# Performance work log

Measured on AMD Instinct MI355X. Metric: run time of the kernel, lower is better.

## Reference

```python
import jax, jax.numpy as jnp
import numpy as np

TOP_K = 2
NUM_MOE_LAYERS = 12


def _gemma_mlp(x, gate_w, up_w, down_w):
    # GemmaMLP: down( gelu_tanh(gate(x)) * up(x) )
    g = jnp.einsum('bsh,hi->bsi', x, gate_w)
    u = jnp.einsum('bsh,hi->bsi', x, up_w)
    return jnp.einsum('bsi,ih->bsh', jax.nn.gelu(g, approximate=True) * u, down_w)


def setup_inputs() -> dict:
    key = jax.random.key(0)
    ks = jax.random.split(key, 8)
    B, S, H, I, E = 32, 256, 1024, 4096, 8  # batch, seq, hidden, intermediate, skill experts
    std = 0.02
    return {
        'x': jax.random.normal(ks[0], (B, S, H), jnp.float32),
        'router_logits': jax.random.normal(ks[1], (B, E), jnp.float32),
        'skill_gate': jax.random.normal(ks[2], (E, H, I), jnp.float32) * std,
        'skill_up': jax.random.normal(ks[3], (E, H, I), jnp.float32) * std,
        'skill_down': jax.random.normal(ks[4], (E, I, H), jnp.float32) * std,
        'shared_gate': jax.random.normal(ks[5], (H, I), jnp.float32) * std,
        'shared_up': jax.random.normal(ks[6], (H, I), jnp.float32) * std,
        'shared_down': jax.random.normal(ks[7], (I, H), jnp.float32) * std,
    }


def reference(x, router_logits, skill_gate, skill_up, skill_down,
              shared_gate, shared_up, shared_down):
    B = x.shape[0]
    E = skill_gate.shape[0]
    # top-k softmax routing (per sequence), renormalized over selected experts
    rw = jax.nn.softmax(router_logits.astype(jnp.float32), axis=-1)
    w, sel = jax.lax.top_k(rw, TOP_K)                      # [B, k]
    w = w / w.sum(axis=-1, keepdims=True)
    w = w.astype(x.dtype)
    # ScaleGradient: identity fwd, grad scaled by 1/num_moe_layers
    scale = 1.0 / NUM_MOE_LAYERS
    w = scale * w + (1.0 - scale) * jax.lax.stop_gradient(w)
    # dense combine weights [B, E]; zero weight == not routed (same math as gather/scatter)
    dense_w = jnp.zeros((B, E), x.dtype).at[jnp.arange(B)[:, None], sel].add(w)

    def step(acc, params):
        g, u, d, we = params                               # we: [B]
        return acc + we[:, None, None] * _gemma_mlp(x, g, u, d), None

    out, _ = jax.lax.scan(step, jnp.zeros_like(x),
                          (skill_gate, skill_up, skill_down, dense_w.T))
    out = out + _gemma_mlp(x, shared_gate, shared_up, shared_down)
    return out
```

## Files before the change

kernel.cpp:

```cpp
#include <hip/hip_runtime.h>

typedef __bf16 bf16x8 __attribute__((ext_vector_type(8)));
typedef float  f32x4  __attribute__((ext_vector_type(4)));

__device__ __forceinline__ unsigned short f2bf(float f) {
    unsigned u = __float_as_uint(f);
    u += 0x7fffu + ((u >> 16) & 1u);
    return (unsigned short)(u >> 16);
}

__device__ __forceinline__ void gld_lds16(const void* g, void* l) {
    __builtin_amdgcn_global_load_lds(
        (const __attribute__((address_space(1))) void*)g,
        (__attribute__((address_space(3))) void*)l,
        16, 0, 0);
}

#define NB  32
#define SQ  256
#define HD  1024
#define ID  4096
#define NEXP 8
#define PAIRS (NB * 3)

#define OFF_EID    ((size_t)0)
#define OFF_WGT    ((size_t)512)
#define OFF_XBF    ((size_t)1024)
#define OFF_GATET  (OFF_XBF   + (size_t)16777216)
#define OFF_UPT    (OFF_GATET + (size_t)75497472)
#define OFF_DOWNT  (OFF_UPT   + (size_t)75497472)
#define OFF_ACT    (OFF_DOWNT + (size_t)75497472)

__global__ void routing_kernel(const float* __restrict__ logits,
                               int* __restrict__ eid, float* __restrict__ wgt) {
    int b = threadIdx.x;
    if (b < NB) {
        float l[NEXP];
        for (int j = 0; j < NEXP; ++j) l[j] = logits[b * NEXP + j];
        int a0 = 0;
        for (int j = 1; j < NEXP; ++j) if (l[j] > l[a0]) a0 = j;
        int a1 = -1;
        for (int j = 0; j < NEXP; ++j) {
            if (j == a0) continue;
            if (a1 < 0 || l[j] > l[a1]) a1 = j;
        }
        float w0 = 1.0f / (1.0f + expf(l[a1] - l[a0]));
        eid[b * 3 + 0] = a0;  wgt[b * 3 + 0] = w0;
        eid[b * 3 + 1] = a1;  wgt[b * 3 + 1] = 1.0f - w0;
        eid[b * 3 + 2] = NEXP; wgt[b * 3 + 2] = 1.0f;
    }
}

__global__ void xcvt_kernel(const float* __restrict__ x,
                            unsigned short* __restrict__ xb, int n4) {
    int i = blockIdx.x * 256 + threadIdx.x;
    if (i < n4) {
        float4 v = ((const float4*)x)[i];
        union { unsigned short s[4]; uint2 u; } p;
        p.s[0] = f2bf(v.x); p.s[1] = f2bf(v.y);
        p.s[2] = f2bf(v.z); p.s[3] = f2bf(v.w);
        ((uint2*)xb)[i] = p.u;
    }
}

__global__ void transpose_cvt(const float* __restrict__ skill,
                              const float* __restrict__ shared_m,
                              unsigned short* __restrict__ out, int R, int C) {
    const int e = blockIdx.z;
    const float* src = (e < NEXP) ? (skill + (size_t)e * R * C) : shared_m;
    unsigned short* dst = out + (size_t)e * R * C;
    const int c0 = blockIdx.x * 64;
    const int r0 = blockIdx.y * 64;
    __shared__ unsigned short t[64][66];
    const int tid = threadIdx.x;
    const int lr = tid >> 4;
    const int lc = (tid & 15) * 4;
    for (int it = 0; it < 4; ++it) {
        int r = lr + it * 16;
        float4 v = *(const float4*)(src + (size_t)(r0 + r) * C + c0 + lc);
        t[r][lc + 0] = f2bf(v.x);
        t[r][lc + 1] = f2bf(v.y);
        t[r][lc + 2] = f2bf(v.z);
        t[r][lc + 3] = f2bf(v.w);
    }
    __syncthreads();
    const int oc = tid >> 2;
    const int k0 = (tid & 3) * 16;
    unsigned int pk[8];
    for (int j = 0; j < 8; ++j) {
        unsigned int lo = t[k0 + 2 * j + 0][oc];
        unsigned int hi = t[k0 + 2 * j + 1][oc];
        pk[j] = lo | (hi << 16);
    }
    unsigned short* dp = dst + (size_t)(c0 + oc) * R + r0 + k0;
    ((uint4*)dp)[0] = make_uint4(pk[0], pk[1], pk[2], pk[3]);
    ((uint4*)dp)[1] = make_uint4(pk[4], pk[5], pk[6], pk[7]);
}

__global__ __launch_bounds__(256, 2) void stage1_gateup(
    const unsigned short* __restrict__ xbf,
    const unsigned short* __restrict__ gateT,
    const unsigned short* __restrict__ upT,
    const int* __restrict__ eid, const float* __restrict__ wgt,
    unsigned short* __restrict__ act)
{
    const int nt = blockIdx.x;
    const int mt = blockIdx.y;
    const int p  = blockIdx.z;
    const int b  = p / 3;
    const int e  = eid[p];
    const float w = wgt[p];

    __shared__ __align__(16) unsigned short lds[3 * 128 * 64];
    unsigned short* La = lds;
    unsigned short* Lg = lds + 8192;
    unsigned short* Lu = lds + 16384;

    const int tid  = threadIdx.x;
    const int wave = tid >> 6;
    const int lane = tid & 63;
    const int wm = (wave >> 1) * 64;
    const int wn = (wave & 1) * 64;

    const unsigned short* Abase = xbf   + (size_t)(b * SQ + mt * 128) * HD;
    const unsigned short* Gbase = gateT + ((size_t)e * ID + nt * 128) * HD;
    const unsigned short* Ubase = upT   + ((size_t)e * ID + nt * 128) * HD;

    const int srow = lane >> 3;
    const int scol = (lane & 7) * 8;

    f32x4 accg[4][4], accu[4][4];
    for (int i = 0; i < 4; ++i)
        for (int j = 0; j < 4; ++j) { accg[i][j] = (f32x4)0.f; accu[i][j] = (f32x4)0.f; }

    const int lrow = lane & 15;
    const int kq   = (lane >> 4) * 8;

    for (int k0 = 0; k0 < HD; k0 += 64) {
        for (int q = 0; q < 4; ++q) {
            const int seg = wave * 4 + q;
            const size_t roff = (size_t)(seg * 8 + srow);
            gld_lds16(Abase + roff * HD + k0 + scol, La + seg * 512);
            gld_lds16(Gbase + roff * HD + k0 + scol, Lg + seg * 512);
            gld_lds16(Ubase + roff * HD + k0 + scol, Lu + seg * 512);
        }
        __syncthreads();
        for (int kk = 0; kk < 64; kk += 32) {
            bf16x8 af[4], gf[4], uf[4];
            for (int mf = 0; mf < 4; ++mf)
                af[mf] = *(const bf16x8*)(La + (wm + mf * 16 + lrow) * 64 + kk + kq);
            for (int nf = 0; nf < 4; ++nf) {
                gf[nf] = *(const bf16x8*)(Lg + (wn + nf * 16 + lrow) * 64 + kk + kq);
                uf[nf] = *(const bf16x8*)(Lu + (wn + nf * 16 + lrow) * 64 + kk + kq);
            }
            for (int mf = 0; mf < 4; ++mf)
                for (int nf = 0; nf < 4; ++nf) {
                    accg[mf][nf] = __builtin_amdgcn_mfma_f32_16x16x32_bf16(af[mf], gf[nf], accg[mf][nf], 0, 0, 0);
                    accu[mf][nf] = __builtin_amdgcn_mfma_f32_16x16x32_bf16(af[mf], uf[nf], accu[mf][nf], 0, 0, 0);
                }
        }
        __syncthreads();
    }

    unsigned short* actp = act + (size_t)p * (SQ * ID);
    const int rb = mt * 128 + wm + ((lane >> 4) << 2);
    const int cb = nt * 128 + wn + (lane & 15);
    for (int mf = 0; mf < 4; ++mf)
        for (int nf = 0; nf < 4; ++nf)
            for (int r = 0; r < 4; ++r) {
                float g = accg[mf][nf][r];
                float u = accu[mf][nf][r];
                float t = 0.7978845608028654f * (g + 0.044715f * g * g * g);
                float h = 0.5f * g * (1.0f + tanhf(t)) * u * w;
                actp[(size_t)(rb + mf * 16 + r) * ID + cb + nf * 16] = f2bf(h);
            }
}

__global__ __launch_bounds__(256, 2) void stage2_down(
    const unsigned short* __restrict__ act,
    const unsigned short* __restrict__ downT,
    const int* __restrict__ eid,
    float* __restrict__ out)
{
    const int nt = blockIdx.x;
    const int mt = blockIdx.y;
    const int b  = blockIdx.z;

    __shared__ __align__(16) unsigned short lds[2 * 128 * 64];
    unsigned short* La = lds;
    unsigned short* Lb = lds + 8192;

    const int tid  = threadIdx.x;
    const int wave = tid >> 6;
    const int lane = tid & 63;
    const int wm = (wave >> 1) * 64;
    const int wn = (wave & 1) * 64;

    const int e0 = eid[b * 3 + 0], e1 = eid[b * 3 + 1], e2 = eid[b * 3 + 2];

    const int srow = lane >> 3;
    const int scol = (lane & 7) * 8;
    const int lrow = lane & 15;
    const int kq   = (lane >> 4) * 8;

    f32x4 acc[4][4];
    for (int i = 0; i < 4; ++i)
        for (int j = 0; j < 4; ++j) acc[i][j] = (f32x4)0.f;

    for (int k0 = 0; k0 < 3 * ID; k0 += 64) {
        const int slot = k0 >> 12;
        const int i0   = k0 & (ID - 1);
        const int e    = (slot == 0) ? e0 : (slot == 1 ? e1 : e2);
        const unsigned short* Abase = act   + ((size_t)(b * 3 + slot) * SQ + mt * 128) * ID + i0;
        const unsigned short* Bbase = downT + ((size_t)e * HD + nt * 128) * ID + i0;
        for (int q = 0; q < 4; ++q) {
            const int seg = wave * 4 + q;
            const size_t roff = (size_t)(seg * 8 + srow);
            gld_lds16(Abase + roff * ID + scol, La + seg * 512);
            gld_lds16(Bbase + roff * ID + scol, Lb + seg * 512);
        }
        __syncthreads();
        for (int kk = 0; kk < 64; kk += 32) {
            bf16x8 af[4], bf[4];
            for (int mf = 0; mf < 4; ++mf)
                af[mf] = *(const bf16x8*)(La + (wm + mf * 16 + lrow) * 64 + kk + kq);
            for (int nf = 0; nf < 4; ++nf)
                bf[nf] = *(const bf16x8*)(Lb + (wn + nf * 16 + lrow) * 64 + kk + kq);
            for (int mf = 0; mf < 4; ++mf)
                for (int nf = 0; nf < 4; ++nf)
                    acc[mf][nf] = __builtin_amdgcn_mfma_f32_16x16x32_bf16(af[mf], bf[nf], acc[mf][nf], 0, 0, 0);
        }
        __syncthreads();
    }

    const int rb = mt * 128 + wm + ((lane >> 4) << 2);
    const int cb = nt * 128 + wn + (lane & 15);
    for (int mf = 0; mf < 4; ++mf)
        for (int nf = 0; nf < 4; ++nf)
            for (int r = 0; r < 4; ++r)
                out[((size_t)b * SQ + rb + mf * 16 + r) * HD + cb + nf * 16] = acc[mf][nf][r];
}

extern "C" void kernel_launch(void* const* d_in, const int* in_sizes, int n_in,
                              void* d_out, int out_size, void* d_ws, size_t ws_size,
                              hipStream_t stream) {
    const float* x        = (const float*)d_in[0];
    const float* logits   = (const float*)d_in[1];
    const float* sk_gate  = (const float*)d_in[2];
    const float* sk_up    = (const float*)d_in[3];
    const float* sk_down  = (const float*)d_in[4];
    const float* sh_gate  = (const float*)d_in[5];
    const float* sh_up    = (const float*)d_in[6];
    const float* sh_down  = (const float*)d_in[7];
    float* out = (float*)d_out;

    char* ws = (char*)d_ws;
    int*            eid   = (int*)(ws + OFF_EID);
    float*          wgt   = (float*)(ws + OFF_WGT);
    unsigned short* xbf   = (unsigned short*)(ws + OFF_XBF);
    unsigned short* gateT = (unsigned short*)(ws + OFF_GATET);
    unsigned short* upT   = (unsigned short*)(ws + OFF_UPT);
    unsigned short* downT = (unsigned short*)(ws + OFF_DOWNT);
    unsigned short* act   = (unsigned short*)(ws + OFF_ACT);

    routing_kernel<<<1, 64, 0, stream>>>(logits, eid, wgt);

    const int n4 = (NB * SQ * HD) / 4;
    xcvt_kernel<<<(n4 + 255) / 256, 256, 0, stream>>>(x, xbf, n4);

    transpose_cvt<<<dim3(ID / 64, HD / 64, 9), 256, 0, stream>>>(sk_gate, sh_gate, gateT, HD, ID);
    transpose_cvt<<<dim3(ID / 64, HD / 64, 9), 256, 0, stream>>>(sk_up,   sh_up,   upT,   HD, ID);
    transpose_cvt<<<dim3(HD / 64, ID / 64, 9), 256, 0, stream>>>(sk_down, sh_down, downT, ID, HD);

    stage1_gateup<<<dim3(ID / 128, SQ / 128, PAIRS), 256, 0, stream>>>(xbf, gateT, upT, eid, wgt, act);
    stage2_down<<<dim3(HD / 128, SQ / 128, NB), 256, 0, stream>>>(act, downT, eid, out);
}
```

Baseline: 1.307 ms.

## Triple-buffer LDS pipeline with swizzled layout and 8-wave blocks in MoE GEMMs

Both GEMM stages now use 512-thread blocks and a three-stage LDS ring buffer with async global-to-LDS loads issued two tiles ahead, gated by explicit vmcnt waits and s_barrier. The LDS layout gets an XOR column swizzle to avoid bank conflicts. The block index is remapped so consecutive blocks land on different XCDs, and stage2 widens its N tile to 256. The goal is to overlap memory latency with MFMA work. In exchange it uses 144KB of dynamic LDS per block, which caps occupancy, and relies on hand-tuned wait counts being correct.

```diff
diff --git a/kernel.cpp b/kernel.cpp
--- a/kernel.cpp
+++ b/kernel.cpp
@@ -15,6 +15,8 @@
         (__attribute__((address_space(3))) void*)l,
         16, 0, 0);
 }
+
+#define WAITVM(N) asm volatile("s_waitcnt vmcnt(" #N ")" ::: "memory")
 
 #define NB  32
 #define SQ  256
@@ -97,148 +99,302 @@
     ((uint4*)dp)[1] = make_uint4(pk[4], pk[5], pk[6], pk[7]);
 }
 
-__global__ __launch_bounds__(256, 2) void stage1_gateup(
+__global__ __launch_bounds__(512, 2) void stage1_gateup(
     const unsigned short* __restrict__ xbf,
     const unsigned short* __restrict__ gateT,
     const unsigned short* __restrict__ upT,
     const int* __restrict__ eid, const float* __restrict__ wgt,
     unsigned short* __restrict__ act)
 {
-    const int nt = blockIdx.x;
-    const int mt = blockIdx.y;
-    const int p  = blockIdx.z;
-    const int b  = p / 3;
-    const int e  = eid[p];
-    const float w = wgt[p];
-
-    __shared__ __align__(16) unsigned short lds[3 * 128 * 64];
-    unsigned short* La = lds;
-    unsigned short* Lg = lds + 8192;
-    unsigned short* Lu = lds + 16384;
+    extern __shared__ unsigned short lds[];
+
+    const int lid = blockIdx.x;
+    const int swz = (lid & 7) * 768 + (lid >> 3);
+    const int nt  = swz & 31;
+    const int mt  = (swz >> 5) & 1;
+    const int p   = swz >> 6;
+    const int b   = p / 3;
+    const int e   = eid[p];
+    const float wS = wgt[p];
 
     const int tid  = threadIdx.x;
-    const int wave = tid >> 6;
+    const int wv   = tid >> 6;
     const int lane = tid & 63;
-    const int wm = (wave >> 1) * 64;
-    const int wn = (wave & 1) * 64;
-
-    const unsigned short* Abase = xbf   + (size_t)(b * SQ + mt * 128) * HD;
-    const unsigned short* Gbase = gateT + ((size_t)e * ID + nt * 128) * HD;
-    const unsigned short* Ubase = upT   + ((size_t)e * ID + nt * 128) * HD;
-
-    const int srow = lane >> 3;
-    const int scol = (lane & 7) * 8;
-
-    f32x4 accg[4][4], accu[4][4];
-    for (int i = 0; i < 4; ++i)
-        for (int j = 0; j < 4; ++j) { accg[i][j] = (f32x4)0.f; accu[i][j] = (f32x4)0.f; }
+    const int wr   = wv >> 2;
+    const int wc   = wv & 3;
+
+    const int lhi  = lane >> 3;
+    const int llo  = lane & 7;
+    const int csw8 = (llo ^ lhi) * 8;
+    const int w2   = wv * 2;
+
+    const size_t lofs = (size_t)(wv * 16 + lhi) * HD + csw8;
+    const unsigned short* pA = xbf   + (size_t)(b * SQ + mt * 128) * HD + lofs;
+    const unsigned short* pG = gateT + ((size_t)e * ID + nt * 128) * HD + lofs;
+    const unsigned short* pU = upT   + ((size_t)e * ID + nt * 128) * HD + lofs;
 
     const int lrow = lane & 15;
     const int kq   = (lane >> 4) * 8;
-
-    for (int k0 = 0; k0 < HD; k0 += 64) {
-        for (int q = 0; q < 4; ++q) {
-            const int seg = wave * 4 + q;
-            const size_t roff = (size_t)(seg * 8 + srow);
-            gld_lds16(Abase + roff * HD + k0 + scol, La + seg * 512);
-            gld_lds16(Gbase + roff * HD + k0 + scol, Lg + seg * 512);
-            gld_lds16(Ubase + roff * HD + k0 + scol, Lu + seg * 512);
-        }
-        __syncthreads();
-        for (int kk = 0; kk < 64; kk += 32) {
-            bf16x8 af[4], gf[4], uf[4];
-            for (int mf = 0; mf < 4; ++mf)
-                af[mf] = *(const bf16x8*)(La + (wm + mf * 16 + lrow) * 64 + kk + kq);
-            for (int nf = 0; nf < 4; ++nf) {
-                gf[nf] = *(const bf16x8*)(Lg + (wn + nf * 16 + lrow) * 64 + kk + kq);
-                uf[nf] = *(const bf16x8*)(Lu + (wn + nf * 16 + lrow) * 64 + kk + kq);
+    const int xt   = (lrow & 7) << 3;
+    const int c0s  = kq ^ xt;
+    const int c1s  = (32 + kq) ^ xt;
+    const int rA0  = (wr * 64 + lrow) * 64;
+    const int rG0  = (wc * 32 + lrow) * 64;
+
+    f32x4 accg[4][2], accu[4][2];
+#pragma unroll
+    for (int i = 0; i < 4; ++i)
+#pragma unroll
+        for (int j = 0; j < 2; ++j) { accg[i][j] = (f32x4)0.f; accu[i][j] = (f32x4)0.f; }
+
+    const int NT = HD / 64;
+
+#pragma unroll
+    for (int t0 = 0; t0 < 2; ++t0) {
+        unsigned short* Lb = lds + t0 * 24576;
+#pragma unroll
+        for (int q = 0; q < 2; ++q) {
+            const size_t o = (size_t)t0 * 64 + (size_t)q * (8 * HD);
+            gld_lds16(pA + o, Lb +         (w2 + q) * 512);
+            gld_lds16(pG + o, Lb +  8192 + (w2 + q) * 512);
+            gld_lds16(pU + o, Lb + 16384 + (w2 + q) * 512);
+        }
+    }
+
+    int cur = 0, tgt = 2;
+#pragma unroll 1
+    for (int t = 0; t < NT; ++t) {
+        __builtin_amdgcn_sched_barrier(0);
+        unsigned short* Lc = lds + cur * 24576;
+        unsigned short* Lt = lds + tgt * 24576;
+        const bool pf = (t + 2 < NT);
+        const size_t kp = (size_t)(t + 2) * 64;
+        if (pf) {
+            gld_lds16(pA + kp, Lt +         w2 * 512);
+            gld_lds16(pG + kp, Lt +  8192 + w2 * 512);
+            gld_lds16(pU + kp, Lt + 16384 + w2 * 512);
+            WAITVM(9);
+        } else if (t + 1 < NT) {
+            WAITVM(6);
+        } else {
+            WAITVM(0);
+        }
+        __builtin_amdgcn_s_barrier();
+        __builtin_amdgcn_sched_barrier(0);
+
+        {
+            bf16x8 af[4], gf[2], uf[2];
+#pragma unroll
+            for (int mf = 0; mf < 4; ++mf)
+                af[mf] = *(const bf16x8*)(Lc + rA0 + mf * 1024 + c0s);
+#pragma unroll
+            for (int nf = 0; nf < 2; ++nf) {
+                gf[nf] = *(const bf16x8*)(Lc +  8192 + rG0 + nf * 1024 + c0s);
+                uf[nf] = *(const bf16x8*)(Lc + 16384 + rG0 + nf * 1024 + c0s);
             }
-            for (int mf = 0; mf < 4; ++mf)
-                for (int nf = 0; nf < 4; ++nf) {
+            __builtin_amdgcn_s_setprio(1);
+#pragma unroll
+            for (int mf = 0; mf < 4; ++mf)
+#pragma unroll
+                for (int nf = 0; nf < 2; ++nf) {
                     accg[mf][nf] = __builtin_amdgcn_mfma_f32_16x16x32_bf16(af[mf], gf[nf], accg[mf][nf], 0, 0, 0);
                     accu[mf][nf] = __builtin_amdgcn_mfma_f32_16x16x32_bf16(af[mf], uf[nf], accu[mf][nf], 0, 0, 0);
                 }
-        }
-        __syncthreads();
+            __builtin_amdgcn_s_setprio(0);
+        }
+        __builtin_amdgcn_s_barrier();
+
+        {
+            bf16x8 af[4], gf[2], uf[2];
+#pragma unroll
+            for (int mf = 0; mf < 4; ++mf)
+                af[mf] = *(const bf16x8*)(Lc + rA0 + mf * 1024 + c1s);
+#pragma unroll
+            for (int nf = 0; nf < 2; ++nf) {
+                gf[nf] = *(const bf16x8*)(Lc +  8192 + rG0 + nf * 1024 + c1s);
+                uf[nf] = *(const bf16x8*)(Lc + 16384 + rG0 + nf * 1024 + c1s);
+            }
+            if (pf) {
+                gld_lds16(pA + kp + 8 * HD, Lt +         (w2 + 1) * 512);
+                gld_lds16(pG + kp + 8 * HD, Lt +  8192 + (w2 + 1) * 512);
+                gld_lds16(pU + kp + 8 * HD, Lt + 16384 + (w2 + 1) * 512);
+            }
+            __builtin_amdgcn_s_setprio(1);
+#pragma unroll
+            for (int mf = 0; mf < 4; ++mf)
+#pragma unroll
+                for (int nf = 0; nf < 2; ++nf) {
+                    accg[mf][nf] = __builtin_amdgcn_mfma_f32_16x16x32_bf16(af[mf], gf[nf], accg[mf][nf], 0, 0, 0);
+                    accu[mf][nf] = __builtin_amdgcn_mfma_f32_16x16x32_bf16(af[mf], uf[nf], accu[mf][nf], 0, 0, 0);
+                }
+            __builtin_amdgcn_s_setprio(0);
+        }
+        __builtin_amdgcn_s_barrier();
+
+        cur = (cur == 2) ? 0 : cur + 1;
+        tgt = (tgt == 2) ? 0 : tgt + 1;
     }
 
     unsigned short* actp = act + (size_t)p * (SQ * ID);
-    const int rb = mt * 128 + wm + ((lane >> 4) << 2);
-    const int cb = nt * 128 + wn + (lane & 15);
+    const int rb = mt * 128 + wr * 64 + ((lane >> 4) << 2);
+    const int cb = nt * 128 + wc * 32 + (lane & 15);
+#pragma unroll
     for (int mf = 0; mf < 4; ++mf)
-        for (int nf = 0; nf < 4; ++nf)
+#pragma unroll
+        for (int nf = 0; nf < 2; ++nf)
+#pragma unroll
             for (int r = 0; r < 4; ++r) {
                 float g = accg[mf][nf][r];
                 float u = accu[mf][nf][r];
-                float t = 0.7978845608028654f * (g + 0.044715f * g * g * g);
-                float h = 0.5f * g * (1.0f + tanhf(t)) * u * w;
+                float tt = 0.7978845608028654f * (g + 0.044715f * g * g * g);
+                float h = 0.5f * g * (1.0f + tanhf(tt)) * u * wS;
                 actp[(size_t)(rb + mf * 16 + r) * ID + cb + nf * 16] = f2bf(h);
             }
 }
 
-__global__ __launch_bounds__(256, 2) void stage2_down(
+__global__ __launch_bounds__(512, 2) void stage2_down(
     const unsigned short* __restrict__ act,
     const unsigned short* __restrict__ downT,
     const int* __restrict__ eid,
     float* __restrict__ out)
 {
-    const int nt = blockIdx.x;
-    const int mt = blockIdx.y;
-    const int b  = blockIdx.z;
-
-    __shared__ __align__(16) unsigned short lds[2 * 128 * 64];
-    unsigned short* La = lds;
-    unsigned short* Lb = lds + 8192;
+    extern __shared__ unsigned short lds[];
+
+    const int lid = blockIdx.x;
+    const int swz = (lid & 7) * 32 + (lid >> 3);
+    const int nt  = swz & 3;
+    const int mt  = (swz >> 2) & 1;
+    const int b   = swz >> 3;
+    const int b3  = b * 3;
+    const int e0 = eid[b3], e1 = eid[b3 + 1], e2 = eid[b3 + 2];
 
     const int tid  = threadIdx.x;
-    const int wave = tid >> 6;
+    const int wv   = tid >> 6;
     const int lane = tid & 63;
-    const int wm = (wave >> 1) * 64;
-    const int wn = (wave & 1) * 64;
-
-    const int e0 = eid[b * 3 + 0], e1 = eid[b * 3 + 1], e2 = eid[b * 3 + 2];
-
-    const int srow = lane >> 3;
-    const int scol = (lane & 7) * 8;
+    const int wr   = wv >> 2;
+    const int wc   = wv & 3;
+
+    const int lhi  = lane >> 3;
+    const int llo  = lane & 7;
+    const int csw8 = (llo ^ lhi) * 8;
+    const int w2   = wv * 2, w4 = wv * 4;
+
+    const size_t laneA = (size_t)(wv * 16 + lhi) * ID + csw8;
+    const size_t laneB = (size_t)(wv * 32 + lhi) * ID + csw8;
+
     const int lrow = lane & 15;
     const int kq   = (lane >> 4) * 8;
+    const int xt   = (lrow & 7) << 3;
+    const int c0s  = kq ^ xt;
+    const int c1s  = (32 + kq) ^ xt;
+    const int rA0  = (wr * 64 + lrow) * 64;
+    const int rB0  = (wc * 64 + lrow) * 64;
 
     f32x4 acc[4][4];
+#pragma unroll
     for (int i = 0; i < 4; ++i)
+#pragma unroll
         for (int j = 0; j < 4; ++j) acc[i][j] = (f32x4)0.f;
 
-    for (int k0 = 0; k0 < 3 * ID; k0 += 64) {
-        const int slot = k0 >> 12;
-        const int i0   = k0 & (ID - 1);
-        const int e    = (slot == 0) ? e0 : (slot == 1 ? e1 : e2);
-        const unsigned short* Abase = act   + ((size_t)(b * 3 + slot) * SQ + mt * 128) * ID + i0;
-        const unsigned short* Bbase = downT + ((size_t)e * HD + nt * 128) * ID + i0;
-        for (int q = 0; q < 4; ++q) {
-            const int seg = wave * 4 + q;
-            const size_t roff = (size_t)(seg * 8 + srow);
-            gld_lds16(Abase + roff * ID + scol, La + seg * 512);
-            gld_lds16(Bbase + roff * ID + scol, Lb + seg * 512);
-        }
-        __syncthreads();
-        for (int kk = 0; kk < 64; kk += 32) {
-            bf16x8 af[4], bf[4];
-            for (int mf = 0; mf < 4; ++mf)
-                af[mf] = *(const bf16x8*)(La + (wm + mf * 16 + lrow) * 64 + kk + kq);
+    const int NT = 3 * ID / 64;
+
+    auto srcAB = [&](int tt, const unsigned short*& A, const unsigned short*& B) {
+        const int slot = tt >> 6;
+        const int i0   = (tt & 63) << 6;
+        const int esl  = (slot == 0) ? e0 : ((slot == 1) ? e1 : e2);
+        A = act   + ((size_t)(b3 + slot) * SQ + mt * 128) * ID + i0 + laneA;
+        B = downT + ((size_t)esl * HD + nt * 256) * ID + i0 + laneB;
+    };
+
+#pragma unroll
+    for (int t0 = 0; t0 < 2; ++t0) {
+        const unsigned short *A, *B;
+        srcAB(t0, A, B);
+        unsigned short* Lb = lds + t0 * 24576;
+#pragma unroll
+        for (int q = 0; q < 2; ++q)
+            gld_lds16(A + (size_t)q * (8 * ID), Lb + (w2 + q) * 512);
+#pragma unroll
+        for (int q = 0; q < 4; ++q)
+            gld_lds16(B + (size_t)q * (8 * ID), Lb + 8192 + (w4 + q) * 512);
+    }
+
+    int cur = 0, tgt = 2;
+#pragma unroll 1
+    for (int t = 0; t < NT; ++t) {
+        __builtin_amdgcn_sched_barrier(0);
+        unsigned short* Lc = lds + cur * 24576;
+        unsigned short* Lt = lds + tgt * 24576;
+        const bool pf = (t + 2 < NT);
+        const unsigned short *SA = nullptr, *SB = nullptr;
+        if (pf) {
+            srcAB(t + 2, SA, SB);
+            gld_lds16(SA,                    Lt +        w2 * 512);
+            gld_lds16(SA + (size_t)(8 * ID), Lt +        (w2 + 1) * 512);
+            gld_lds16(SB,                    Lt + 8192 + w4 * 512);
+            WAITVM(9);
+        } else if (t + 1 < NT) {
+            WAITVM(6);
+        } else {
+            WAITVM(0);
+        }
+        __builtin_amdgcn_s_barrier();
+        __builtin_amdgcn_sched_barrier(0);
+
+        {
+            bf16x8 af[4], bfr[4];
+#pragma unroll
+            for (int mf = 0; mf < 4; ++mf)
+                af[mf] = *(const bf16x8*)(Lc + rA0 + mf * 1024 + c0s);
+#pragma unroll
             for (int nf = 0; nf < 4; ++nf)
-                bf[nf] = *(const bf16x8*)(Lb + (wn + nf * 16 + lrow) * 64 + kk + kq);
-            for (int mf = 0; mf < 4; ++mf)
+                bfr[nf] = *(const bf16x8*)(Lc + 8192 + rB0 + nf * 1024 + c0s);
+            __builtin_amdgcn_s_setprio(1);
+#pragma unroll
+            for (int mf = 0; mf < 4; ++mf)
+#pragma unroll
                 for (int nf = 0; nf < 4; ++nf)
-                    acc[mf][nf] = __builtin_amdgcn_mfma_f32_16x16x32_bf16(af[mf], bf[nf], acc[mf][nf], 0, 0, 0);
-        }
-        __syncthreads();
-    }
-
-    const int rb = mt * 128 + wm + ((lane >> 4) << 2);
-    const int cb = nt * 128 + wn + (lane & 15);
+                    acc[mf][nf] = __builtin_amdgcn_mfma_f32_16x16x32_bf16(af[mf], bfr[nf], acc[mf][nf], 0, 0, 0);
+            __builtin_amdgcn_s_setprio(0);
+        }
+        __builtin_amdgcn_s_barrier();
+
+        {
+            bf16x8 af[4], bfr[4];
+#pragma unroll
+            for (int mf = 0; mf < 4; ++mf)
+                af[mf] = *(const bf16x8*)(Lc + rA0 + mf * 1024 + c1s);
+#pragma unroll
+            for (int nf = 0; nf < 4; ++nf)
+                bfr[nf] = *(const bf16x8*)(Lc + 8192 + rB0 + nf * 1024 + c1s);
+            if (pf) {
+                gld_lds16(SB + (size_t)(8  * ID), Lt + 8192 + (w4 + 1) * 512);
+                gld_lds16(SB + (size_t)(16 * ID), Lt + 8192 + (w4 + 2) * 512);
+                gld_lds16(SB + (size_t)(24 * ID), Lt + 8192 + (w4 + 3) * 512);
+            }
+            __builtin_amdgcn_s_setprio(1);
+#pragma unroll
+            for (int mf = 0; mf < 4; ++mf)
+#pragma unroll
+                for (int nf = 0; nf < 4; ++nf)
+                    acc[mf][nf] = __builtin_amdgcn_mfma_f32_16x16x32_bf16(af[mf], bfr[nf], acc[mf][nf], 0, 0, 0);
+            __builtin_amdgcn_s_setprio(0);
+        }
+        __builtin_amdgcn_s_barrier();
+
+        cur = (cur == 2) ? 0 : cur + 1;
+        tgt = (tgt == 2) ? 0 : tgt + 1;
+    }
+
+    const int rb  = mt * 128 + wr * 64 + ((lane >> 4) << 2);
+    const int cbN = nt * 256 + wc * 64 + (lane & 15);
+#pragma unroll
     for (int mf = 0; mf < 4; ++mf)
+#pragma unroll
         for (int nf = 0; nf < 4; ++nf)
+#pragma unroll
             for (int r = 0; r < 4; ++r)
-                out[((size_t)b * SQ + rb + mf * 16 + r) * HD + cb + nf * 16] = acc[mf][nf][r];
+                out[((size_t)b * SQ + rb + mf * 16 + r) * HD + cbN + nf * 16] = acc[mf][nf][r];
 }
 
 extern "C" void kernel_launch(void* const* d_in, const int* in_sizes, int n_in,
@@ -263,6 +419,15 @@
     unsigned short* downT = (unsigned short*)(ws + OFF_DOWNT);
     unsigned short* act   = (unsigned short*)(ws + OFF_ACT);
 
+    static int attr_set = 0;
+    if (!attr_set) {
+        hipFuncSetAttribute(reinterpret_cast<const void*>(stage1_gateup),
+                            hipFuncAttributeMaxDynamicSharedMemorySize, 147456);
+        hipFuncSetAttribute(reinterpret_cast<const void*>(stage2_down),
+                            hipFuncAttributeMaxDynamicSharedMemorySize, 147456);
+        attr_set = 1;
+    }
+
     routing_kernel<<<1, 64, 0, stream>>>(logits, eid, wgt);
 
     const int n4 = (NB * SQ * HD) / 4;
@@ -272,6 +437,6 @@
     transpose_cvt<<<dim3(ID / 64, HD / 64, 9), 256, 0, stream>>>(sk_up,   sh_up,   upT,   HD, ID);
     transpose_cvt<<<dim3(HD / 64, ID / 64, 9), 256, 0, stream>>>(sk_down, sh_down, downT, ID, HD);
 
-    stage1_gateup<<<dim3(ID / 128, SQ / 128, PAIRS), 256, 0, stream>>>(xbf, gateT, upT, eid, wgt, act);
-    stage2_down<<<dim3(HD / 128, SQ / 128, NB), 256, 0, stream>>>(act, downT, eid, out);
-}
+    stage1_gateup<<<dim3(PAIRS * 64), 512, 147456, stream>>>(xbf, gateT, upT, eid, wgt, act);
+    stage2_down<<<dim3(256), 512, 147456, stream>>>(act, downT, eid, out);
+}
```

Result: faster. 1.207 ms (-7.6%).
